# Kernel optimization log

Hardware: AMD Instinct MI355X
Metric: run time of the kernel (lower is better)

## Reference

```python
import jax, jax.numpy as jnp
import numpy as np

B, L, A, BD, K, M, FP, R, T = 256, 128, 39, 10, 6, 256, 256, 3, 2


def _gru(x, h, w_ih, w_hh, b_ih, b_hh):
    # PyTorch GRUCell: gates ordered (reset, update, new)
    gi = x @ w_ih.T + b_ih
    gh = h @ w_hh.T + b_hh
    i_r, i_z, i_n = jnp.split(gi, 3, axis=-1)
    h_r, h_z, h_n = jnp.split(gh, 3, axis=-1)
    r = jax.nn.sigmoid(i_r + h_r)
    z = jax.nn.sigmoid(i_z + h_z)
    n = jnp.tanh(i_n + r * h_n)
    return (1.0 - z) * n + z * h


def setup_inputs() -> dict:
    key = jax.random.key(0)
    ks = jax.random.split(key, 26)
    n = lambda i, shape: jax.random.normal(ks[i], shape, jnp.float32) * 0.05
    return dict(
        atom_list=jax.random.normal(ks[0], (B, L, A), jnp.float32),
        bond_list=jax.random.normal(ks[1], (B, M, BD), jnp.float32),
        atom_degree_list=jax.random.randint(ks[2], (B, L, K), 0, L),
        bond_degree_list=jax.random.randint(ks[3], (B, L, K), 0, M),
        atom_mask=jnp.ones((B, L), jnp.float32),
        atom_fc_W=n(4, (FP, A)), atom_fc_b=n(5, (FP,)),
        neighbor_fc_W=n(6, (FP, A + BD)), neighbor_fc_b=n(7, (FP,)),
        gru_w_ih=n(8, (R, 3 * FP, FP)), gru_w_hh=n(9, (R, 3 * FP, FP)),
        gru_b_ih=n(10, (R, 3 * FP)), gru_b_hh=n(11, (R, 3 * FP)),
        align_W=n(12, (R, 1, 2 * FP)), align_b=n(13, (R, 1)),
        attend_W=n(14, (R, FP, FP)), attend_b=n(15, (R, FP)),
        mol_gru_w_ih=n(16, (3 * FP, FP)), mol_gru_w_hh=n(17, (3 * FP, FP)),
        mol_gru_b_ih=n(18, (3 * FP,)), mol_gru_b_hh=n(19, (3 * FP,)),
        mol_align_W=n(20, (1, 2 * FP)), mol_align_b=n(21, (1,)),
        mol_attend_W=n(22, (FP, FP)), mol_attend_b=n(23, (FP,)),
    )


def reference(atom_list, bond_list, atom_degree_list, bond_degree_list, atom_mask,
              atom_fc_W, atom_fc_b, neighbor_fc_W, neighbor_fc_b,
              gru_w_ih, gru_w_hh, gru_b_ih, gru_b_hh,
              align_W, align_b, attend_W, attend_b,
              mol_gru_w_ih, mol_gru_w_hh, mol_gru_b_ih, mol_gru_b_hh,
              mol_align_W, mol_align_b, mol_attend_W, mol_attend_b):
    Bn, Ln, _ = atom_list.shape
    Fp = atom_fc_W.shape[0]
    gather = jax.vmap(lambda t, i: t[i])  # per-batch row gather

    atom_pre = atom_list @ atom_fc_W.T + atom_fc_b          # (B,L,FP) pre-relu
    atom_feature = jax.nn.relu(atom_pre)
    afv = [atom_pre]

    bond_neighbor = gather(bond_list, bond_degree_list)      # (B,L,K,BD)
    atom_neighbor = gather(atom_list, atom_degree_list)      # (B,L,K,A)
    nf = jax.nn.relu(jnp.concatenate([atom_neighbor, bond_neighbor], -1)
                     @ neighbor_fc_W.T + neighbor_fc_b)       # (B,L,K,FP)

    pad = atom_degree_list == Ln - 1                          # padding-atom index
    attend_mask = jnp.where(pad, 0.0, 1.0)[..., None]
    softmax_mask = jnp.where(pad, -9.0, 0.0)[..., None]

    h = atom_feature.reshape(Bn * Ln, Fp)
    act = atom_feature
    awv = []
    for d in range(R):
        neigh = nf if d == 0 else gather(act, atom_degree_list)
        fa = jnp.concatenate(
            [jnp.broadcast_to(act[:, :, None, :], neigh.shape), neigh], -1)
        score = jax.nn.relu(fa @ align_W[d].T + align_b[d]) + softmax_mask
        aw = jax.nn.softmax(score, axis=-2) * attend_mask     # (B,L,K,1)
        awv.append(aw)
        ctx = jax.nn.relu(jnp.sum(aw * (neigh @ attend_W[d].T + attend_b[d]), -2))
        h = _gru(ctx.reshape(Bn * Ln, Fp), h,
                 gru_w_ih[d], gru_w_hh[d], gru_b_ih[d], gru_b_hh[d])
        atom_feature = h.reshape(Bn, Ln, Fp)
        act = jax.nn.relu(atom_feature)
        afv.append(act)

    m3 = atom_mask[..., None]
    mol_unb = [jnp.sum(atom_feature * m3, -2)]
    mol_feature = jnp.sum(act * m3, -2)
    act_mol = jax.nn.relu(mol_feature)
    mfv = [mol_feature]
    mawv = []
    mol_smask = jnp.where(m3 == 0, -9e8, 0.0)
    for _ in range(T):
        ma = jnp.concatenate(
            [jnp.broadcast_to(act_mol[:, None, :], act.shape), act], -1)
        ms = jax.nn.relu(ma @ mol_align_W.T + mol_align_b) + mol_smask
        mw = jax.nn.softmax(ms, axis=-2) * m3                 # (B,L,1)
        mawv.append(mw)
        mctx = jax.nn.relu(jnp.sum(mw * (act @ mol_attend_W.T + mol_attend_b), -2))
        mol_feature = _gru(mctx, mol_feature,
                           mol_gru_w_ih, mol_gru_w_hh, mol_gru_b_ih, mol_gru_b_hh)
        mol_unb.append(mol_feature)
        act_mol = jax.nn.relu(mol_feature)
        mfv.append(act_mol)

    return (atom_feature, jnp.stack(afv), jnp.stack(awv), jnp.stack(mfv),
            jnp.stack(mol_unb), jnp.stack(mawv), mol_feature)
```

## Files before the change

kernel.cpp:

```cpp
#include <hip/hip_runtime.h>
#include <hip/hip_bf16.h>

#define BB 256
#define LL 128
#define AA 39
#define BDD 10
#define KK 6
#define MM 256
#define FP 256
#define RR 3
#define TT 2

using short8  = __attribute__((ext_vector_type(8))) short;
using short4v = __attribute__((ext_vector_type(4))) short;
using f32x4   = __attribute__((ext_vector_type(4))) float;
using f32x2   = __attribute__((ext_vector_type(2))) float;

__device__ __forceinline__ short f2bf(float f) {
    union { float f; unsigned u; } v; v.f = f;
    unsigned u = v.u;
    u += 0x7fffu + ((u >> 16) & 1u);
    return (short)(u >> 16);
}
__device__ __forceinline__ float bf2f(short s) {
    union { unsigned u; float f; } v; v.u = ((unsigned)(unsigned short)s) << 16;
    return v.f;
}
__device__ __forceinline__ float wred64(float v) {
#pragma unroll
    for (int off = 32; off >= 1; off >>= 1) v += __shfl_xor(v, off);
    return v;
}

#define GLL(gp, lp) __builtin_amdgcn_global_load_lds( \
    (const __attribute__((address_space(1))) void*)(gp), \
    (__attribute__((address_space(3))) void*)(lp), 16, 0, 0)

__global__ __launch_bounds__(256) void k_transpose(const float* __restrict__ src,
                                                   float* __restrict__ dst, int O, int I) {
    int idx = blockIdx.x * 256 + threadIdx.x;
    if (idx >= O * I) return;
    int o = idx / I, i = idx - o * I;
    dst[i * O + o] = src[idx];
}

__global__ __launch_bounds__(256) void k_prep_gruw(const float* __restrict__ gwih,
                                                   const float* __restrict__ gwhh,
                                                   short* __restrict__ out) {
    int idx = blockIdx.x * 256 + threadIdx.x;
    if (idx >= RR * 2 * 8 * 48 * 512) return;
    int j = idx & 7;
    int lane = (idx >> 3) & 63;
    int blk = idx >> 9;
    int nt = blk % 48;
    int ks = (blk / 48) % 8;
    int mat = (blk / (48 * 8)) % 2;
    int d = blk / (48 * 8 * 2);
    int n = nt * 16 + (lane & 15);
    int k = ks * 32 + (lane >> 4) * 8 + j;
    const float* W = mat ? gwhh : gwih;
    out[idx] = f2bf(W[((size_t)d * 768 + n) * FP + k]);
}

__global__ __launch_bounds__(256) void k_prep_molfrag(const float* __restrict__ mih,
                                                      const float* __restrict__ mhh,
                                                      short* __restrict__ out) {
    int idx = blockIdx.x * 256 + threadIdx.x;
    if (idx >= 2 * 8 * 48 * 512) return;
    int j = idx & 7;
    int lane = (idx >> 3) & 63;
    int blk = idx >> 9;
    int nt = blk % 48;
    int ks = (blk / 48) % 8;
    int mat = blk / (48 * 8);
    int n = nt * 16 + (lane & 15);
    int k = ks * 32 + (lane >> 4) * 8 + j;
    const float* W = mat ? mhh : mih;
    out[idx] = f2bf(W[(size_t)n * FP + k]);
}

__global__ __launch_bounds__(256) void k_prep_waf(const float* __restrict__ atW,
                                                  short* __restrict__ out) {
    int idx = blockIdx.x * 256 + threadIdx.x;
    if (idx >= RR * 8 * 16 * 512) return;
    int j = idx & 7;
    int lane = (idx >> 3) & 63;
    int blk = idx >> 9;
    int nt = blk % 16;
    int ks = (blk / 16) % 8;
    int d = blk / 128;
    int n = nt * 16 + (lane & 15);
    int k = ks * 32 + (lane >> 4) * 8 + j;
    out[idx] = f2bf(atW[(size_t)d * FP * FP + (size_t)n * FP + k]);
}

__global__ __launch_bounds__(256) void k_atom_pre(const float* __restrict__ atom_list,
                                                  const float* __restrict__ WafcT,
                                                  const float* __restrict__ afc_b,
                                                  const float* __restrict__ WnT,
                                                  const float* __restrict__ bn,
                                                  float* __restrict__ out_pre,
                                                  short* __restrict__ hb16,
                                                  short* __restrict__ ApreB) {
    int g0 = blockIdx.x * 8;
    int t = threadIdx.x;
    __shared__ float x[8][AA];
    for (int i = t; i < 8 * AA; i += 256) x[i / AA][i % AA] = atom_list[(size_t)g0 * AA + i];
    __syncthreads();
    float a1[8], a2[8];
    float b1 = afc_b[t], b2 = bn[t];
#pragma unroll
    for (int a = 0; a < 8; ++a) { a1[a] = b1; a2[a] = b2; }
    for (int i = 0; i < AA; ++i) {
        float w1 = WafcT[i * FP + t];
        float w2 = WnT[i * FP + t];
#pragma unroll
        for (int a = 0; a < 8; ++a) { a1[a] += x[a][i] * w1; a2[a] += x[a][i] * w2; }
    }
#pragma unroll
    for (int a = 0; a < 8; ++a) {
        size_t idx = (size_t)(g0 + a) * FP + t;
        out_pre[idx] = a1[a];
        hb16[idx] = f2bf(fmaxf(a1[a], 0.f));
        ApreB[idx] = f2bf(a2[a]);
    }
}

__global__ __launch_bounds__(512) void k_actx_d0(
        const short* __restrict__ ACTB,
        const short* __restrict__ ApreB,
        const float* __restrict__ bond_list,
        const int* __restrict__ adeg, const int* __restrict__ bdeg,
        const float* __restrict__ WnT,
        const float* __restrict__ alW, const float* __restrict__ alb,
        const short* __restrict__ WaF, const float* __restrict__ atb,
        short* __restrict__ ctx_out, float* __restrict__ awv_out) {
    __shared__ __align__(16) short aS[32768];
    __shared__ __align__(16) short cS[32768];
    __shared__ int jxS[LL * KK];
    __shared__ int bxS[LL * KK];
    __shared__ float swS[LL];

    const int b = blockIdx.x;
    const int t = threadIdx.x;
    const int wave = t >> 6, lane = t & 63;
    const int lr = lane & 15, lk = lane >> 4;

#define SLAB_OFF(r, cb) ((((r) * 512 + (cb))) ^ ((((r) & 7)) << 4))
#define A4R(r, c)  (*(const short4v*)((const char*)aS + SLAB_OFF(r, (c) * 2)))
#define C8R(r, c)  (*(const short8*)((const char*)cS + SLAB_OFF(r, (c) * 2)))
#define CW4(r, c, v) (*(short4v*)((char*)cS + SLAB_OFF(r, (c) * 2)) = (v))

    {
        const char* src = (const char*)(ApreB + (size_t)b * LL * FP);
#pragma unroll
        for (int it = 0; it < 8; ++it) {
            int off = it * 8192 + wave * 1024 + lane * 16;
            int so = off ^ (((off >> 9) & 7) << 4);
            GLL(src + so, (char*)aS + off);
        }
        for (int i = t; i < LL * KK; i += 512) {
            jxS[i] = adeg[b * LL * KK + i];
            bxS[i] = bdeg[b * LL * KK + i];
        }
    }

    f32x4 w0 = *(const f32x4*)(alW + lane * 4);
    f32x4 w1 = *(const f32x4*)(alW + FP + lane * 4);
    float bias = alb[0];

    float wnt[BDD][4];
#pragma unroll
    for (int i = 0; i < BDD; ++i) {
        f32x4 v = *(const f32x4*)(WnT + (AA + i) * FP + lane * 4);
#pragma unroll
        for (int q = 0; q < 4; ++q) wnt[i][q] = v[q];
    }
    __syncthreads();

    for (int ai = 0; ai < 16; ++ai) {
        const int a = wave * 16 + ai;
        const int ga = b * LL + a;

        short4v sv = *(const short4v*)(ACTB + (size_t)ga * FP + lane * 4);
        float ss = wred64(bf2f(sv[0]) * w0[0] + bf2f(sv[1]) * w0[1] +
                          bf2f(sv[2]) * w0[2] + bf2f(sv[3]) * w0[3]);

        int jx[KK];
#pragma unroll
        for (int k = 0; k < KK; ++k) jx[k] = jxS[a * KK + k];

        float nf[KK][4];
        float sc[KK];
#pragma unroll
        for (int k = 0; k < KK; ++k) {
            short4v nv = A4R(jx[k], lane * 4);
            float f0 = bf2f(nv[0]), f1 = bf2f(nv[1]), f2 = bf2f(nv[2]), f3 = bf2f(nv[3]);
            int bi = bxS[a * KK + k];
            const float* bp = bond_list + ((size_t)b * MM + bi) * BDD;
            float bb[BDD];
#pragma unroll
            for (int i = 0; i < 5; ++i) {
                f32x2 v2 = *(const f32x2*)(bp + 2 * i);
                bb[2 * i] = v2[0]; bb[2 * i + 1] = v2[1];
            }
            float b0 = 0.f, b1 = 0.f, b2 = 0.f, b3 = 0.f;
#pragma unroll
            for (int i = 0; i < BDD; ++i) {
                b0 += bb[i] * wnt[i][0]; b1 += bb[i] * wnt[i][1];
                b2 += bb[i] * wnt[i][2]; b3 += bb[i] * wnt[i][3];
            }
            f0 = fmaxf(f0 + b0, 0.f); f1 = fmaxf(f1 + b1, 0.f);
            f2 = fmaxf(f2 + b2, 0.f); f3 = fmaxf(f3 + b3, 0.f);
            nf[k][0] = f0; nf[k][1] = f1; nf[k][2] = f2; nf[k][3] = f3;
            float s2 = wred64(f0 * w1[0] + f1 * w1[1] + f2 * w1[2] + f3 * w1[3]);
            float s = fmaxf(ss + s2 + bias, 0.f);
            if (jx[k] == LL - 1) s -= 9.0f;
            sc[k] = s;
        }

        float m = sc[0];
#pragma unroll
        for (int k = 1; k < KK; ++k) m = fmaxf(m, sc[k]);
        float e[KK], den = 0.f;
#pragma unroll
        for (int k = 0; k < KK; ++k) { e[k] = expf(sc[k] - m); den += e[k]; }
        float aw[KK], sumaw = 0.f;
#pragma unroll
        for (int k = 0; k < KK; ++k) {
            aw[k] = (jx[k] == LL - 1) ? 0.f : e[k] / den;
            sumaw += aw[k];
        }
        if (lane < KK) {
            float av = aw[0];
#pragma unroll
            for (int k = 1; k < KK; ++k) if (lane == k) av = aw[k];
            awv_out[(size_t)ga * KK + lane] = av;
        }
        if (lane == 0) swS[a] = sumaw;

        short4v wo;
#pragma unroll
        for (int q = 0; q < 4; ++q) {
            float w = 0.f;
#pragma unroll
            for (int k = 0; k < KK; ++k) w += aw[k] * nf[k][q];
            wo[q] = f2bf(w);
        }
        CW4(a, lane * 4, wo);
    }
    __syncthreads();

    {
        const int rg = wave >> 1, csl = wave & 1;
        f32x4 acc[2][8] = {};
        const short8* wb = (const short8*)WaF;
        for (int ks = 0; ks < 8; ++ks) {
            short8 a0 = C8R(rg * 32 + lr, ks * 32 + lk * 8);
            short8 a1 = C8R(rg * 32 + 16 + lr, ks * 32 + lk * 8);
#pragma unroll
            for (int nt2 = 0; nt2 < 8; ++nt2) {
                short8 bf = wb[(size_t)(ks * 16 + csl * 8 + nt2) * 64 + lane];
                acc[0][nt2] = __builtin_amdgcn_mfma_f32_16x16x32_bf16(a0, bf, acc[0][nt2], 0, 0, 0);
                acc[1][nt2] = __builtin_amdgcn_mfma_f32_16x16x32_bf16(a1, bf, acc[1][nt2], 0, 0, 0);
            }
        }
#pragma unroll
        for (int rt = 0; rt < 2; ++rt)
#pragma unroll
        for (int nt2 = 0; nt2 < 8; ++nt2) {
            int col = csl * 128 + nt2 * 16 + lr;
            float abv = atb[col];
#pragma unroll
            for (int q = 0; q < 4; ++q) {
                int row = rg * 32 + rt * 16 + lk * 4 + q;
                float v = acc[rt][nt2][q] + swS[row] * abv;
                ctx_out[((size_t)b * LL + row) * FP + col] = f2bf(fmaxf(v, 0.f));
            }
        }
    }
#undef SLAB_OFF
#undef A4R
#undef C8R
#undef CW4
}

__global__ __launch_bounds__(512) void k_actx(int d,
        const short* __restrict__ ACTB,
        const int* __restrict__ adeg,
        const float* __restrict__ alW, const float* __restrict__ alb,
        const short* __restrict__ WaF, const float* __restrict__ atb,
        short* __restrict__ ctx_out, float* __restrict__ awv_out) {
    __shared__ __align__(16) short aS[32768];
    __shared__ __align__(16) short cS[32768];
    __shared__ int   jxS[LL * KK];
    __shared__ float awS[LL * KK];
    __shared__ float swS[LL];

    const int b = blockIdx.x;
    const int t = threadIdx.x;
    const int wave = t >> 6, lane = t & 63;
    const int lr = lane & 15, lk = lane >> 4;

#define SLAB_OFF(r, cb) ((((r) * 512 + (cb))) ^ ((((r) & 7)) << 4))
#define A4R(r, c)  (*(const short4v*)((const char*)aS + SLAB_OFF(r, (c) * 2)))
#define C8R(r, c)  (*(const short8*)((const char*)cS + SLAB_OFF(r, (c) * 2)))
#define CW4(r, c, v) (*(short4v*)((char*)cS + SLAB_OFF(r, (c) * 2)) = (v))

    {
        const char* src = (const char*)(ACTB + (size_t)b * LL * FP);
#pragma unroll
        for (int it = 0; it < 8; ++it) {
            int off = it * 8192 + wave * 1024 + lane * 16;
            int so = off ^ (((off >> 9) & 7) << 4);
            GLL(src + so, (char*)aS + off);
        }
        for (int i = t; i < LL * KK; i += 512) jxS[i] = adeg[b * LL * KK + i];
    }
    __syncthreads();

    {
        f32x4 w0 = *(const f32x4*)(alW + (size_t)d * 2 * FP + lane * 4);
        f32x4 w1 = *(const f32x4*)(alW + (size_t)d * 2 * FP + FP + lane * 4);
        float bias = alb[d];
        for (int ai = 0; ai < 16; ++ai) {
            int a = wave * 16 + ai;
            short4v sv = A4R(a, lane * 4);
            float ss = wred64(bf2f(sv[0]) * w0[0] + bf2f(sv[1]) * w0[1] +
                              bf2f(sv[2]) * w0[2] + bf2f(sv[3]) * w0[3]);
            float sc[KK]; int jx[KK];
#pragma unroll
            for (int k = 0; k < KK; ++k) {
                int j = jxS[a * KK + k]; jx[k] = j;
                short4v nv = A4R(j, lane * 4);
                float s2 = wred64(bf2f(nv[0]) * w1[0] + bf2f(nv[1]) * w1[1] +
                                  bf2f(nv[2]) * w1[2] + bf2f(nv[3]) * w1[3]);
                float s = fmaxf(ss + s2 + bias, 0.f);
                if (j == LL - 1) s -= 9.0f;
                sc[k] = s;
            }
            float m = sc[0];
#pragma unroll
            for (int k = 1; k < KK; ++k) m = fmaxf(m, sc[k]);
            float e[KK], den = 0.f;
#pragma unroll
            for (int k = 0; k < KK; ++k) { e[k] = expf(sc[k] - m); den += e[k]; }
            float aw[KK], sumaw = 0.f;
#pragma unroll
            for (int k = 0; k < KK; ++k) {
                aw[k] = (jx[k] == LL - 1) ? 0.f : e[k] / den;
                sumaw += aw[k];
            }
            if (lane < KK) {
                float av = aw[0];
#pragma unroll
                for (int k = 1; k < KK; ++k) if (lane == k) av = aw[k];
                awS[a * KK + lane] = av;
                awv_out[((size_t)b * LL + a) * KK + lane] = av;
            }
            if (lane == 0) swS[a] = sumaw;
        }
    }
    __syncthreads();

    for (int ai = 0; ai < 16; ++ai) {
        int a = wave * 16 + ai;
        float a0 = 0.f, a1 = 0.f, a2 = 0.f, a3 = 0.f;
#pragma unroll
        for (int k = 0; k < KK; ++k) {
            float awv = awS[a * KK + k];
            short4v nv = A4R(jxS[a * KK + k], lane * 4);
            a0 += awv * bf2f(nv[0]);
            a1 += awv * bf2f(nv[1]);
            a2 += awv * bf2f(nv[2]);
            a3 += awv * bf2f(nv[3]);
        }
        short4v wo; wo[0] = f2bf(a0); wo[1] = f2bf(a1); wo[2] = f2bf(a2); wo[3] = f2bf(a3);
        CW4(a, lane * 4, wo);
    }
    __syncthreads();

    {
        const int rg = wave >> 1, csl = wave & 1;
        f32x4 acc[2][8] = {};
        const short8* wb = (const short8*)(WaF + (size_t)d * 8 * 16 * 512);
        for (int ks = 0; ks < 8; ++ks) {
            short8 a0 = C8R(rg * 32 + lr, ks * 32 + lk * 8);
            short8 a1 = C8R(rg * 32 + 16 + lr, ks * 32 + lk * 8);
#pragma unroll
            for (int nt2 = 0; nt2 < 8; ++nt2) {
                short8 bf = wb[(size_t)(ks * 16 + csl * 8 + nt2) * 64 + lane];
                acc[0][nt2] = __builtin_amdgcn_mfma_f32_16x16x32_bf16(a0, bf, acc[0][nt2], 0, 0, 0);
                acc[1][nt2] = __builtin_amdgcn_mfma_f32_16x16x32_bf16(a1, bf, acc[1][nt2], 0, 0, 0);
            }
        }
#pragma unroll
        for (int rt = 0; rt < 2; ++rt)
#pragma unroll
        for (int nt2 = 0; nt2 < 8; ++nt2) {
            int col = csl * 128 + nt2 * 16 + lr;
            float abv = atb[d * FP + col];
#pragma unroll
            for (int q = 0; q < 4; ++q) {
                int row = rg * 32 + rt * 16 + lk * 4 + q;
                float v = acc[rt][nt2][q] + swS[row] * abv;
                ctx_out[((size_t)b * LL + row) * FP + col] = f2bf(fmaxf(v, 0.f));
            }
        }
    }
#undef SLAB_OFF
#undef A4R
#undef C8R
#undef CW4
}

template<int LAST>
__global__ __launch_bounds__(512) void k_gru_mfma(
        const short* __restrict__ XB,
        const short* __restrict__ HBl,
        float* __restrict__ hbuf,
        const short* __restrict__ Bih,
        const short* __restrict__ Bhh,
        const float* __restrict__ bih, const float* __restrict__ bhh,
        float* __restrict__ act_out,
        short* __restrict__ HB_out,
        short* __restrict__ ACT_out) {
    __shared__ short ldsB[3][12288];
    __shared__ short ldsA[2][16384];
    const int t = threadIdx.x;
    const int wave = t >> 6, lane = t & 63;
    const int rh = wave >> 2;
    const int wn = wave & 3;
    const int lr = lane & 15, lk = lane >> 4;
    const int bid = blockIdx.x;
    const int kofs = bid & 7;
    const int abase = bid * 64;

#define PKS(p)  ((((p) >> 2) + kofs) & 7)
#define STAGEP(p) do { \
        const short* base_ = ((((p) >> 1) & 1) ? Bhh : Bih) + (size_t)PKS(p) * 24576; \
        const int h_ = (p) & 1; \
        _Pragma("unroll") \
        for (int e = 0; e < 3; ++e) { \
            int j = wave * 3 + e; \
            int nt = 4 * (j >> 1) + 2 * h_ + (j & 1); \
            GLL(base_ + nt * 512 + lane * 8, &ldsB[(p) % 3][j * 512]); \
        } } while (0)
#define LDA_READ(s, r, c) (*(const short8*)((const char*)ldsA[s] + \
        ((((r) * 512 + (c) * 2)) ^ ((((r) & 7)) << 4))))
#define LDA_READ1(s, r, c) (*(const short*)((const char*)ldsA[s] + \
        ((((r) * 512 + (c) * 2)) ^ ((((r) & 7)) << 4))))

    {
        const char* xsrc = (const char*)(XB + (size_t)abase * FP);
        const char* hsrc = (const char*)(HBl + (size_t)abase * FP);
#pragma unroll
        for (int it = 0; it < 4; ++it) {
            int off = it * 8192 + wave * 1024 + lane * 16;
            int src = off ^ (((off >> 9) & 7) << 4);
            GLL(xsrc + src, (char*)ldsA[0] + off);
            GLL(hsrc + src, (char*)ldsA[1] + off);
        }
    }
    STAGEP(0);
    STAGEP(1);

    f32x4 acc_rz[2][8] = {};
    f32x4 acc_in[2][4] = {};
    f32x4 acc_hn[2][4] = {};

    short8 ax0{}, ah0{}, ax1{}, ah1{};
#pragma unroll
    for (int p = 0; p < 32; ++p) {
        if (p < 31) { asm volatile("s_waitcnt vmcnt(3)" ::: "memory"); }
        else        { asm volatile("s_waitcnt vmcnt(0)" ::: "memory"); }
        __builtin_amdgcn_s_barrier();
        __builtin_amdgcn_sched_barrier(0);
        if (p < 30) STAGEP(p + 2);
        const int h_ = p & 1;
        const int mat = (p >> 1) & 1;
        if ((p & 3) == 0) {
            int ks = PKS(p);
            int c = ks * 32 + lk * 8;
            ax0 = LDA_READ(0, rh * 32 + lr, c);
            ah0 = LDA_READ(1, rh * 32 + lr, c);
            ax1 = LDA_READ(0, rh * 32 + 16 + lr, c);
            ah1 = LDA_READ(1, rh * 32 + 16 + lr, c);
        }
#pragma unroll
        for (int rg = 0; rg < 2; ++rg) {
            const short8 a8 = mat ? (rg ? ah1 : ah0) : (rg ? ax1 : ax0);
#pragma unroll
            for (int g = 0; g < 3; ++g) {
#pragma unroll
                for (int s2 = 0; s2 < 2; ++s2) {
                    const int sub = 2 * h_ + s2;
                    const int j = ((4 * g + wn) << 1) | s2;
                    short8 bf = *(const short8*)(&ldsB[p % 3][j * 512 + lane * 8]);
                    if (g < 2)
                        acc_rz[rg][g * 4 + sub] = __builtin_amdgcn_mfma_f32_16x16x32_bf16(a8, bf, acc_rz[rg][g * 4 + sub], 0, 0, 0);
                    else if (mat)
                        acc_hn[rg][sub] = __builtin_amdgcn_mfma_f32_16x16x32_bf16(a8, bf, acc_hn[rg][sub], 0, 0, 0);
                    else
                        acc_in[rg][sub] = __builtin_amdgcn_mfma_f32_16x16x32_bf16(a8, bf, acc_in[rg][sub], 0, 0, 0);
                }
            }
        }
    }
#undef STAGEP
#undef PKS

#pragma unroll
    for (int sub = 0; sub < 4; ++sub) {
        int c = wn * 64 + sub * 16 + lr;
        float brz_r = bih[c] + bhh[c];
        float brz_z = bih[FP + c] + bhh[FP + c];
        float bin_ = bih[2 * FP + c];
        float bhn = bhh[2 * FP + c];
#pragma unroll
        for (int rg = 0; rg < 2; ++rg) {
#pragma unroll
            for (int q = 0; q < 4; ++q) {
                int row = rh * 32 + rg * 16 + lk * 4 + q;
                int atom = abase + row;
                size_t idx = (size_t)atom * FP + c;
                float hold = bf2f(LDA_READ1(1, row, c));
                float r = 1.f / (1.f + expf(-(acc_rz[rg][0 * 4 + sub][q] + brz_r)));
                float z = 1.f / (1.f + expf(-(acc_rz[rg][1 * 4 + sub][q] + brz_z)));
                float n = tanhf(acc_in[rg][sub][q] + bin_ + r * (acc_hn[rg][sub][q] + bhn));
                float hn = (1.f - z) * n + z * hold;
                float rl = fmaxf(hn, 0.f);
                act_out[idx] = rl;
                if constexpr (LAST) {
                    hbuf[idx] = hn;
                } else {
                    HB_out[idx] = f2bf(hn);
                    ACT_out[idx] = f2bf(rl);
                }
            }
        }
    }
#undef LDA_READ
#undef LDA_READ1
}

__global__ __launch_bounds__(256) void k_mol_reduce(const float* __restrict__ hbuf,
                                                    const float* __restrict__ act,
                                                    const float* __restrict__ mask,
                                                    const float* __restrict__ malW,
                                                    float* __restrict__ o_unb0,
                                                    float* __restrict__ o_mfv0,
                                                    float* __restrict__ molF,
                                                    short* __restrict__ MOLFb,
                                                    float* __restrict__ S2g) {
    int b = blockIdx.x, t = threadIdx.x;
    int wave = t >> 6, lane = t & 63;
    float s1 = 0.f, s2 = 0.f;
    for (int l = 0; l < LL; ++l) {
        float mk = mask[b * LL + l];
        s1 += hbuf[((size_t)b * LL + l) * FP + t] * mk;
        s2 += act[((size_t)b * LL + l) * FP + t] * mk;
    }
    o_unb0[b * FP + t] = s1;
    o_mfv0[b * FP + t] = s2;
    molF[b * FP + t] = s2;
    MOLFb[b * FP + t] = f2bf(s2);

    for (int l = wave; l < LL; l += 4) {
        float v2 = 0.f;
#pragma unroll
        for (int q = 0; q < 4; ++q) {
            int i = lane + 64 * q;
            v2 += act[((size_t)b * LL + l) * FP + i] * malW[FP + i];
        }
        v2 = wred64(v2);
        if (lane == 0) S2g[b * LL + l] = v2;
    }
}

__global__ __launch_bounds__(256) void k_mstep(int step,
        const float* __restrict__ act,
        const float* __restrict__ molF,
        const float* __restrict__ mask,
        const float* __restrict__ S2g,
        const float* __restrict__ malW, const float* __restrict__ malb,
        const float* __restrict__ MWaT, const float* __restrict__ matb,
        short* __restrict__ MCTXb,
        float* __restrict__ o_mawv) {
    int b = blockIdx.x, t = threadIdx.x;
    int wave = t >> 6, lane = t & 63;
    __shared__ float sS[LL], mwS[LL], waS[FP];
    __shared__ float red[4];

    float hprev = molF[b * FP + t];
    float am = fmaxf(hprev, 0.f);

    float v = am * malW[t];
    v = wred64(v);
    if (lane == 0) red[wave] = v;
    __syncthreads();
    float s_self = red[0] + red[1] + red[2] + red[3];

    if (t < LL) {
        float s = fmaxf(s_self + S2g[b * LL + t] + malb[0], 0.f);
        if (mask[b * LL + t] == 0.f) s += -9e8f;
        sS[t] = s;
    }
    __syncthreads();

    float m = -1e30f;
    for (int l = 0; l < LL; ++l) m = fmaxf(m, sS[l]);
    float den = 0.f;
    for (int l = 0; l < LL; ++l) den += expf(sS[l] - m);
    if (t < LL) {
        float w = expf(sS[t] - m) / den * mask[b * LL + t];
        mwS[t] = w;
        o_mawv[(size_t)step * (BB * LL) + b * LL + t] = w;
    }
    __syncthreads();

    float sumaw = 0.f;
    for (int l = 0; l < LL; ++l) sumaw += mwS[l];

    float wa = 0.f;
    for (int l = 0; l < LL; ++l) wa += mwS[l] * act[((size_t)b * LL + l) * FP + t];
    waS[t] = wa;
    __syncthreads();

    float acc = sumaw * matb[t];
    for (int i = 0; i < FP; ++i) acc += waS[i] * MWaT[i * FP + t];
    MCTXb[b * FP + t] = f2bf(fmaxf(acc, 0.f));
}

__global__ __launch_bounds__(512) void k_mol_gru(int step,
        const short* __restrict__ XB,
        const short* __restrict__ HBl,
        const short* __restrict__ Bih,
        const short* __restrict__ Bhh,
        const float* __restrict__ bih, const float* __restrict__ bhh,
        float* __restrict__ o_unb, float* __restrict__ o_mfv,
        float* __restrict__ molF, short* __restrict__ MOLFb,
        float* __restrict__ o_molfeat) {
    __shared__ short ldsB[3][12288];
    __shared__ short ldsA[2][16384];
    const int t = threadIdx.x;
    const int wave = t >> 6, lane = t & 63;
    const int rh = wave >> 2;
    const int wn = wave & 3;
    const int lr = lane & 15, lk = lane >> 4;
    const int bid = blockIdx.x;
    const int kofs = bid & 7;
    const int abase = bid * 64;

#define PKS(p)  ((((p) >> 2) + kofs) & 7)
#define STAGEP(p) do { \
        const short* base_ = ((((p) >> 1) & 1) ? Bhh : Bih) + (size_t)PKS(p) * 24576; \
        const int h_ = (p) & 1; \
        _Pragma("unroll") \
        for (int e = 0; e < 3; ++e) { \
            int j = wave * 3 + e; \
            int nt = 4 * (j >> 1) + 2 * h_ + (j & 1); \
            GLL(base_ + nt * 512 + lane * 8, &ldsB[(p) % 3][j * 512]); \
        } } while (0)
#define LDA_READ(s, r, c) (*(const short8*)((const char*)ldsA[s] + \
        ((((r) * 512 + (c) * 2)) ^ ((((r) & 7)) << 4))))
#define LDA_READ1(s, r, c) (*(const short*)((const char*)ldsA[s] + \
        ((((r) * 512 + (c) * 2)) ^ ((((r) & 7)) << 4))))

    {
        const char* xsrc = (const char*)(XB + (size_t)abase * FP);
        const char* hsrc = (const char*)(HBl + (size_t)abase * FP);
#pragma unroll
        for (int it = 0; it < 4; ++it) {
            int off = it * 8192 + wave * 1024 + lane * 16;
            int src = off ^ (((off >> 9) & 7) << 4);
            GLL(xsrc + src, (char*)ldsA[0] + off);
            GLL(hsrc + src, (char*)ldsA[1] + off);
        }
    }
    STAGEP(0);
    STAGEP(1);

    f32x4 acc_rz[2][8] = {};
    f32x4 acc_in[2][4] = {};
    f32x4 acc_hn[2][4] = {};

    short8 ax0{}, ah0{}, ax1{}, ah1{};
#pragma unroll
    for (int p = 0; p < 32; ++p) {
        if (p < 31) { asm volatile("s_waitcnt vmcnt(3)" ::: "memory"); }
        else        { asm volatile("s_waitcnt vmcnt(0)" ::: "memory"); }
        __builtin_amdgcn_s_barrier();
        __builtin_amdgcn_sched_barrier(0);
        if (p < 30) STAGEP(p + 2);
        const int h_ = p & 1;
        const int mat = (p >> 1) & 1;
        if ((p & 3) == 0) {
            int ks = PKS(p);
            int c = ks * 32 + lk * 8;
            ax0 = LDA_READ(0, rh * 32 + lr, c);
            ah0 = LDA_READ(1, rh * 32 + lr, c);
            ax1 = LDA_READ(0, rh * 32 + 16 + lr, c);
            ah1 = LDA_READ(1, rh * 32 + 16 + lr, c);
        }
#pragma unroll
        for (int rg = 0; rg < 2; ++rg) {
            const short8 a8 = mat ? (rg ? ah1 : ah0) : (rg ? ax1 : ax0);
#pragma unroll
            for (int g = 0; g < 3; ++g) {
#pragma unroll
                for (int s2 = 0; s2 < 2; ++s2) {
                    const int sub = 2 * h_ + s2;
                    const int j = ((4 * g + wn) << 1) | s2;
                    short8 bf = *(const short8*)(&ldsB[p % 3][j * 512 + lane * 8]);
                    if (g < 2)
                        acc_rz[rg][g * 4 + sub] = __builtin_amdgcn_mfma_f32_16x16x32_bf16(a8, bf, acc_rz[rg][g * 4 + sub], 0, 0, 0);
                    else if (mat)
                        acc_hn[rg][sub] = __builtin_amdgcn_mfma_f32_16x16x32_bf16(a8, bf, acc_hn[rg][sub], 0, 0, 0);
                    else
                        acc_in[rg][sub] = __builtin_amdgcn_mfma_f32_16x16x32_bf16(a8, bf, acc_in[rg][sub], 0, 0, 0);
                }
            }
        }
    }
#undef STAGEP
#undef PKS

#pragma unroll
    for (int sub = 0; sub < 4; ++sub) {
        int c = wn * 64 + sub * 16 + lr;
        float brz_r = bih[c] + bhh[c];
        float brz_z = bih[FP + c] + bhh[FP + c];
        float bin_ = bih[2 * FP + c];
        float bhn = bhh[2 * FP + c];
#pragma unroll
        for (int rg = 0; rg < 2; ++rg) {
#pragma unroll
            for (int q = 0; q < 4; ++q) {
                int row = rh * 32 + rg * 16 + lk * 4 + q;
                int m = abase + row;
                size_t idx = (size_t)m * FP + c;
                float hold = bf2f(LDA_READ1(1, row, c));
                float r = 1.f / (1.f + expf(-(acc_rz[rg][0 * 4 + sub][q] + brz_r)));
                float z = 1.f / (1.f + expf(-(acc_rz[rg][1 * 4 + sub][q] + brz_z)));
                float n = tanhf(acc_in[rg][sub][q] + bin_ + r * (acc_hn[rg][sub][q] + bhn));
                float hn = (1.f - z) * n + z * hold;
                o_unb[(size_t)(step + 1) * (BB * FP) + idx] = hn;
                o_mfv[(size_t)(step + 1) * (BB * FP) + idx] = fmaxf(hn, 0.f);
                molF[idx] = hn;
                MOLFb[idx] = f2bf(hn);
                if (step == TT - 1) o_molfeat[idx] = hn;
            }
        }
    }
#undef LDA_READ
#undef LDA_READ1
}

extern "C" void kernel_launch(void* const* d_in, const int* in_sizes, int n_in,
                              void* d_out, int out_size, void* d_ws, size_t ws_size,
                              hipStream_t stream) {
    const float* atom_list = (const float*)d_in[0];
    const float* bond_list = (const float*)d_in[1];
    const int*   adeg      = (const int*)d_in[2];
    const int*   bdeg      = (const int*)d_in[3];
    const float* amask     = (const float*)d_in[4];
    const float* atom_fc_W = (const float*)d_in[5];
    const float* atom_fc_b = (const float*)d_in[6];
    const float* nfc_W     = (const float*)d_in[7];
    const float* nfc_b     = (const float*)d_in[8];
    const float* gwih      = (const float*)d_in[9];
    const float* gwhh      = (const float*)d_in[10];
    const float* gbih      = (const float*)d_in[11];
    const float* gbhh      = (const float*)d_in[12];
    const float* alW       = (const float*)d_in[13];
    const float* alb       = (const float*)d_in[14];
    const float* atW       = (const float*)d_in[15];
    const float* atb       = (const float*)d_in[16];
    const float* mgwih     = (const float*)d_in[17];
    const float* mgwhh     = (const float*)d_in[18];
    const float* mgbih     = (const float*)d_in[19];
    const float* mgbhh     = (const float*)d_in[20];
    const float* malW      = (const float*)d_in[21];
    const float* malb      = (const float*)d_in[22];
    const float* matW      = (const float*)d_in[23];
    const float* matb      = (const float*)d_in[24];

    const size_t BLF = (size_t)BB * LL * FP;
    float* out = (float*)d_out;
    float* O0 = out;
    float* O1 = out + BLF;
    float* O2 = O1 + 4 * BLF;
    float* O3 = O2 + (size_t)RR * BB * LL * KK;
    float* O4 = O3 + (size_t)(TT + 1) * BB * FP;
    float* O5 = O4 + (size_t)(TT + 1) * BB * FP;
    float* O6 = O5 + (size_t)TT * BB * LL;

    float* ws = (float*)d_ws;
    short* XB   = (short*)ws;
    short* XB2  = XB + BLF;
    short* HBb  = XB + 2 * BLF;
    short* ACTB = XB + 3 * BLF;
    float* rest = ws + 2 * BLF;
    short* ApreB = (short*)rest;
    float* SW    = rest + BLF / 2;
    float* MOLF  = SW + (size_t)BB * LL;
    float* WafcT = MOLF + (size_t)BB * FP;
    float* WnT   = WafcT + AA * FP;
    float* MWaT  = WnT + (AA + BDD) * FP;
    short* MolGW = (short*)(MWaT + (size_t)FP * FP);
    short* GW    = MolGW + (size_t)2 * 8 * 48 * 512;
    short* WaF   = GW + (size_t)RR * 2 * 8 * 48 * 512;
    short* MCTXb = WaF + (size_t)RR * 8 * 16 * 512;
    short* MOLFb = MCTXb + (size_t)BB * FP;
    float* S2g   = (float*)(MOLFb + (size_t)BB * FP);
    (void)ws_size; (void)in_sizes; (void)n_in; (void)out_size;

    auto tr = [&](const float* src, float* dst, int O, int I) {
        int n = O * I;
        k_transpose<<<(n + 255) / 256, 256, 0, stream>>>(src, dst, O, I);
    };
    tr(atom_fc_W, WafcT, FP, AA);
    tr(nfc_W, WnT, FP, AA + BDD);
    tr(matW, MWaT, FP, FP);

    {
        int n = RR * 2 * 8 * 48 * 512;
        k_prep_gruw<<<(n + 255) / 256, 256, 0, stream>>>(gwih, gwhh, GW);
        int n2 = RR * 8 * 16 * 512;
        k_prep_waf<<<(n2 + 255) / 256, 256, 0, stream>>>(atW, WaF);
        int n3 = 2 * 8 * 48 * 512;
        k_prep_molfrag<<<(n3 + 255) / 256, 256, 0, stream>>>(mgwih, mgwhh, MolGW);
    }

    k_atom_pre<<<BB * LL / 8, 256, 0, stream>>>(atom_list, WafcT, atom_fc_b,
                                                WnT, nfc_b, O1, HBb, ApreB);

    const size_t wblk = (size_t)8 * 48 * 512;
    for (int d = 0; d < RR; ++d) {
        if (d == 0) {
            k_actx_d0<<<BB, 512, 0, stream>>>(HBb, ApreB, bond_list, adeg, bdeg,
                    WnT, alW, alb, WaF, atb, XB2, O2);
        } else {
            k_actx<<<BB, 512, 0, stream>>>(d, ACTB, adeg,
                    alW, alb, WaF, atb,
                    XB2, O2 + (size_t)d * BB * LL * KK);
        }
        if (d == RR - 1) {
            k_gru_mfma<1><<<BB * LL / 64, 512, 0, stream>>>(XB2, HBb, O0,
                    GW + (size_t)(d * 2 + 0) * wblk, GW + (size_t)(d * 2 + 1) * wblk,
                    gbih + (size_t)d * 768, gbhh + (size_t)d * 768,
                    O1 + (size_t)(d + 1) * BLF, HBb, ACTB);
        } else {
            k_gru_mfma<0><<<BB * LL / 64, 512, 0, stream>>>(XB2, HBb, O0,
                    GW + (size_t)(d * 2 + 0) * wblk, GW + (size_t)(d * 2 + 1) * wblk,
                    gbih + (size_t)d * 768, gbhh + (size_t)d * 768,
                    O1 + (size_t)(d + 1) * BLF, HBb, ACTB);
        }
    }

    const float* actFin = O1 + (size_t)RR * BLF;
    k_mol_reduce<<<BB, 256, 0, stream>>>(O0, actFin, amask, malW,
                                         O4, O3, MOLF, MOLFb, S2g);
    for (int st = 0; st < TT; ++st) {
        k_mstep<<<BB, 256, 0, stream>>>(st, actFin, MOLF, amask, S2g,
                malW, malb, MWaT, matb, MCTXb, O5);
        k_mol_gru<<<4, 512, 0, stream>>>(st, MCTXb, MOLFb,
                MolGW, MolGW + wblk, mgbih, mgbhh,
                O4, O3, MOLF, MOLFb, O6);
    }
}
```

Baseline: 541.2 us.

## Fuse prep kernels, merge actx attention passes, fold first mol step into reduce

Merges the three transpose launches into one and the three weight-pack launches into one. In k_actx, alignment softmax and weighted neighbor sum now run in a single pass, keeping neighbor rows in registers instead of re-reading LDS and dropping the awS buffer and one barrier. The first molecule attention step is folded into the reduce kernel, which removes one launch. Fewer launches and less LDS traffic in exchange for higher register pressure and a serial per-block tail in the mol head.

```diff
diff --git a/kernel.cpp b/kernel.cpp
--- a/kernel.cpp
+++ b/kernel.cpp
@@ -36,62 +36,58 @@
     (const __attribute__((address_space(1))) void*)(gp), \
     (__attribute__((address_space(3))) void*)(lp), 16, 0, 0)
 
-__global__ __launch_bounds__(256) void k_transpose(const float* __restrict__ src,
-                                                   float* __restrict__ dst, int O, int I) {
+__global__ __launch_bounds__(256) void k_prep_trans(
+        const float* __restrict__ atom_fc_W, const float* __restrict__ nfc_W,
+        const float* __restrict__ matW,
+        float* __restrict__ WafcT, float* __restrict__ WnT, float* __restrict__ MWaT) {
+    const int N1 = FP * AA, N2 = FP * (AA + BDD), N3 = FP * FP;
     int idx = blockIdx.x * 256 + threadIdx.x;
-    if (idx >= O * I) return;
-    int o = idx / I, i = idx - o * I;
-    dst[i * O + o] = src[idx];
-}
-
-__global__ __launch_bounds__(256) void k_prep_gruw(const float* __restrict__ gwih,
-                                                   const float* __restrict__ gwhh,
-                                                   short* __restrict__ out) {
+    if (idx < N1) {
+        int o = idx / AA, i = idx - o * AA;
+        WafcT[i * FP + o] = atom_fc_W[idx];
+    } else if (idx < N1 + N2) {
+        int r = idx - N1;
+        int o = r / (AA + BDD), i = r - o * (AA + BDD);
+        WnT[i * FP + o] = nfc_W[r];
+    } else if (idx < N1 + N2 + N3) {
+        int r = idx - N1 - N2;
+        int o = r >> 8, i = r & 255;
+        MWaT[i * FP + o] = matW[r];
+    }
+}
+
+__global__ __launch_bounds__(256) void k_prep_pack(
+        const float* __restrict__ gwih, const float* __restrict__ gwhh,
+        const float* __restrict__ atW,
+        const float* __restrict__ mih, const float* __restrict__ mhh,
+        short* __restrict__ GW, short* __restrict__ WaF, short* __restrict__ MolGW) {
+    const int N1 = RR * 2 * 8 * 48 * 512;
+    const int N2 = RR * 8 * 16 * 512;
+    const int N3 = 2 * 8 * 48 * 512;
     int idx = blockIdx.x * 256 + threadIdx.x;
-    if (idx >= RR * 2 * 8 * 48 * 512) return;
-    int j = idx & 7;
-    int lane = (idx >> 3) & 63;
-    int blk = idx >> 9;
-    int nt = blk % 48;
-    int ks = (blk / 48) % 8;
-    int mat = (blk / (48 * 8)) % 2;
-    int d = blk / (48 * 8 * 2);
-    int n = nt * 16 + (lane & 15);
-    int k = ks * 32 + (lane >> 4) * 8 + j;
-    const float* W = mat ? gwhh : gwih;
-    out[idx] = f2bf(W[((size_t)d * 768 + n) * FP + k]);
-}
-
-__global__ __launch_bounds__(256) void k_prep_molfrag(const float* __restrict__ mih,
-                                                      const float* __restrict__ mhh,
-                                                      short* __restrict__ out) {
-    int idx = blockIdx.x * 256 + threadIdx.x;
-    if (idx >= 2 * 8 * 48 * 512) return;
-    int j = idx & 7;
-    int lane = (idx >> 3) & 63;
-    int blk = idx >> 9;
-    int nt = blk % 48;
-    int ks = (blk / 48) % 8;
-    int mat = blk / (48 * 8);
-    int n = nt * 16 + (lane & 15);
-    int k = ks * 32 + (lane >> 4) * 8 + j;
-    const float* W = mat ? mhh : mih;
-    out[idx] = f2bf(W[(size_t)n * FP + k]);
-}
-
-__global__ __launch_bounds__(256) void k_prep_waf(const float* __restrict__ atW,
-                                                  short* __restrict__ out) {
-    int idx = blockIdx.x * 256 + threadIdx.x;
-    if (idx >= RR * 8 * 16 * 512) return;
-    int j = idx & 7;
-    int lane = (idx >> 3) & 63;
-    int blk = idx >> 9;
-    int nt = blk % 16;
-    int ks = (blk / 16) % 8;
-    int d = blk / 128;
-    int n = nt * 16 + (lane & 15);
-    int k = ks * 32 + (lane >> 4) * 8 + j;
-    out[idx] = f2bf(atW[(size_t)d * FP * FP + (size_t)n * FP + k]);
+    if (idx < N1) {
+        int j = idx & 7, lane = (idx >> 3) & 63, blk = idx >> 9;
+        int nt = blk % 48, ks = (blk / 48) % 8, mat = (blk / 384) % 2, d = blk / 768;
+        int n = nt * 16 + (lane & 15);
+        int k = ks * 32 + (lane >> 4) * 8 + j;
+        const float* W = mat ? gwhh : gwih;
+        GW[idx] = f2bf(W[((size_t)d * 768 + n) * FP + k]);
+    } else if (idx < N1 + N2) {
+        int r = idx - N1;
+        int j = r & 7, lane = (r >> 3) & 63, blk = r >> 9;
+        int nt = blk % 16, ks = (blk / 16) % 8, d = blk / 128;
+        int n = nt * 16 + (lane & 15);
+        int k = ks * 32 + (lane >> 4) * 8 + j;
+        WaF[r] = f2bf(atW[(size_t)d * FP * FP + (size_t)n * FP + k]);
+    } else if (idx < N1 + N2 + N3) {
+        int r = idx - N1 - N2;
+        int j = r & 7, lane = (r >> 3) & 63, blk = r >> 9;
+        int nt = blk % 48, ks = (blk / 48) % 8, mat = blk / 384;
+        int n = nt * 16 + (lane & 15);
+        int k = ks * 32 + (lane >> 4) * 8 + j;
+        const float* W = mat ? mhh : mih;
+        MolGW[r] = f2bf(W[(size_t)n * FP + k]);
+    }
 }
 
 __global__ __launch_bounds__(256) void k_atom_pre(const float* __restrict__ atom_list,
@@ -294,7 +290,6 @@
     __shared__ __align__(16) short aS[32768];
     __shared__ __align__(16) short cS[32768];
     __shared__ int   jxS[LL * KK];
-    __shared__ float awS[LL * KK];
     __shared__ float swS[LL];
 
     const int b = blockIdx.x;
@@ -317,65 +312,66 @@
         }
         for (int i = t; i < LL * KK; i += 512) jxS[i] = adeg[b * LL * KK + i];
     }
-    __syncthreads();
-
-    {
-        f32x4 w0 = *(const f32x4*)(alW + (size_t)d * 2 * FP + lane * 4);
-        f32x4 w1 = *(const f32x4*)(alW + (size_t)d * 2 * FP + FP + lane * 4);
-        float bias = alb[d];
-        for (int ai = 0; ai < 16; ++ai) {
-            int a = wave * 16 + ai;
-            short4v sv = A4R(a, lane * 4);
-            float ss = wred64(bf2f(sv[0]) * w0[0] + bf2f(sv[1]) * w0[1] +
-                              bf2f(sv[2]) * w0[2] + bf2f(sv[3]) * w0[3]);
-            float sc[KK]; int jx[KK];
-#pragma unroll
-            for (int k = 0; k < KK; ++k) {
-                int j = jxS[a * KK + k]; jx[k] = j;
-                short4v nv = A4R(j, lane * 4);
-                float s2 = wred64(bf2f(nv[0]) * w1[0] + bf2f(nv[1]) * w1[1] +
-                                  bf2f(nv[2]) * w1[2] + bf2f(nv[3]) * w1[3]);
-                float s = fmaxf(ss + s2 + bias, 0.f);
-                if (j == LL - 1) s -= 9.0f;
-                sc[k] = s;
-            }
-            float m = sc[0];
-#pragma unroll
-            for (int k = 1; k < KK; ++k) m = fmaxf(m, sc[k]);
-            float e[KK], den = 0.f;
-#pragma unroll
-            for (int k = 0; k < KK; ++k) { e[k] = expf(sc[k] - m); den += e[k]; }
-            float aw[KK], sumaw = 0.f;
-#pragma unroll
-            for (int k = 0; k < KK; ++k) {
-                aw[k] = (jx[k] == LL - 1) ? 0.f : e[k] / den;
-                sumaw += aw[k];
-            }
-            if (lane < KK) {
-                float av = aw[0];
-#pragma unroll
-                for (int k = 1; k < KK; ++k) if (lane == k) av = aw[k];
-                awS[a * KK + lane] = av;
-                awv_out[((size_t)b * LL + a) * KK + lane] = av;
-            }
-            if (lane == 0) swS[a] = sumaw;
-        }
-    }
+
+    f32x4 w0 = *(const f32x4*)(alW + (size_t)d * 2 * FP + lane * 4);
+    f32x4 w1 = *(const f32x4*)(alW + (size_t)d * 2 * FP + FP + lane * 4);
+    float bias = alb[d];
     __syncthreads();
 
     for (int ai = 0; ai < 16; ++ai) {
-        int a = wave * 16 + ai;
-        float a0 = 0.f, a1 = 0.f, a2 = 0.f, a3 = 0.f;
+        const int a = wave * 16 + ai;
+        const int ga = b * LL + a;
+
+        short4v sv = A4R(a, lane * 4);
+        float ss = wred64(bf2f(sv[0]) * w0[0] + bf2f(sv[1]) * w0[1] +
+                          bf2f(sv[2]) * w0[2] + bf2f(sv[3]) * w0[3]);
+
+        int jx[KK];
+#pragma unroll
+        for (int k = 0; k < KK; ++k) jx[k] = jxS[a * KK + k];
+
+        float nf[KK][4];
+        float sc[KK];
 #pragma unroll
         for (int k = 0; k < KK; ++k) {
-            float awv = awS[a * KK + k];
-            short4v nv = A4R(jxS[a * KK + k], lane * 4);
-            a0 += awv * bf2f(nv[0]);
-            a1 += awv * bf2f(nv[1]);
-            a2 += awv * bf2f(nv[2]);
-            a3 += awv * bf2f(nv[3]);
-        }
-        short4v wo; wo[0] = f2bf(a0); wo[1] = f2bf(a1); wo[2] = f2bf(a2); wo[3] = f2bf(a3);
+            short4v nv = A4R(jx[k], lane * 4);
+            nf[k][0] = bf2f(nv[0]); nf[k][1] = bf2f(nv[1]);
+            nf[k][2] = bf2f(nv[2]); nf[k][3] = bf2f(nv[3]);
+            float s2 = wred64(nf[k][0] * w1[0] + nf[k][1] * w1[1] +
+                              nf[k][2] * w1[2] + nf[k][3] * w1[3]);
+            float s = fmaxf(ss + s2 + bias, 0.f);
+            if (jx[k] == LL - 1) s -= 9.0f;
+            sc[k] = s;
+        }
+
+        float m = sc[0];
+#pragma unroll
+        for (int k = 1; k < KK; ++k) m = fmaxf(m, sc[k]);
+        float e[KK], den = 0.f;
+#pragma unroll
+        for (int k = 0; k < KK; ++k) { e[k] = expf(sc[k] - m); den += e[k]; }
+        float aw[KK], sumaw = 0.f;
+#pragma unroll
+        for (int k = 0; k < KK; ++k) {
+            aw[k] = (jx[k] == LL - 1) ? 0.f : e[k] / den;
+            sumaw += aw[k];
+        }
+        if (lane < KK) {
+            float av = aw[0];
+#pragma unroll
+            for (int k = 1; k < KK; ++k) if (lane == k) av = aw[k];
+            awv_out[(size_t)ga * KK + lane] = av;
+        }
+        if (lane == 0) swS[a] = sumaw;
+
+        short4v wo;
+#pragma unroll
+        for (int q = 0; q < 4; ++q) {
+            float w = 0.f;
+#pragma unroll
+            for (int k = 0; k < KK; ++k) w += aw[k] * nf[k][q];
+            wo[q] = f2bf(w);
+        }
         CW4(a, lane * 4, wo);
     }
     __syncthreads();
@@ -544,17 +540,20 @@
 #undef LDA_READ1
 }
 
-__global__ __launch_bounds__(256) void k_mol_reduce(const float* __restrict__ hbuf,
-                                                    const float* __restrict__ act,
-                                                    const float* __restrict__ mask,
-                                                    const float* __restrict__ malW,
-                                                    float* __restrict__ o_unb0,
-                                                    float* __restrict__ o_mfv0,
-                                                    float* __restrict__ molF,
-                                                    short* __restrict__ MOLFb,
-                                                    float* __restrict__ S2g) {
+__global__ __launch_bounds__(256) void k_mol_head(
+        const float* __restrict__ hbuf, const float* __restrict__ act,
+        const float* __restrict__ mask,
+        const float* __restrict__ malW, const float* __restrict__ malb,
+        const float* __restrict__ MWaT, const float* __restrict__ matb,
+        float* __restrict__ o_unb0, float* __restrict__ o_mfv0,
+        float* __restrict__ molF, short* __restrict__ MOLFb,
+        float* __restrict__ S2g,
+        short* __restrict__ MCTXb, float* __restrict__ o_mawv) {
     int b = blockIdx.x, t = threadIdx.x;
     int wave = t >> 6, lane = t & 63;
+    __shared__ float sS2[LL], sS[LL], mwS[LL], waS[FP];
+    __shared__ float red[4];
+
     float s1 = 0.f, s2 = 0.f;
     for (int l = 0; l < LL; ++l) {
         float mk = mask[b * LL + l];
@@ -574,8 +573,45 @@
             v2 += act[((size_t)b * LL + l) * FP + i] * malW[FP + i];
         }
         v2 = wred64(v2);
-        if (lane == 0) S2g[b * LL + l] = v2;
-    }
+        if (lane == 0) { sS2[l] = v2; S2g[b * LL + l] = v2; }
+    }
+
+    float am = fmaxf(s2, 0.f);
+    float v = am * malW[t];
+    v = wred64(v);
+    if (lane == 0) red[wave] = v;
+    __syncthreads();
+    float s_self = red[0] + red[1] + red[2] + red[3];
+
+    if (t < LL) {
+        float s = fmaxf(s_self + sS2[t] + malb[0], 0.f);
+        if (mask[b * LL + t] == 0.f) s += -9e8f;
+        sS[t] = s;
+    }
+    __syncthreads();
+
+    float m = -1e30f;
+    for (int l = 0; l < LL; ++l) m = fmaxf(m, sS[l]);
+    float den = 0.f;
+    for (int l = 0; l < LL; ++l) den += expf(sS[l] - m);
+    if (t < LL) {
+        float w = expf(sS[t] - m) / den * mask[b * LL + t];
+        mwS[t] = w;
+        o_mawv[b * LL + t] = w;
+    }
+    __syncthreads();
+
+    float sumaw = 0.f;
+    for (int l = 0; l < LL; ++l) sumaw += mwS[l];
+
+    float wa = 0.f;
+    for (int l = 0; l < LL; ++l) wa += mwS[l] * act[((size_t)b * LL + l) * FP + t];
+    waS[t] = wa;
+    __syncthreads();
+
+    float acc = sumaw * matb[t];
+    for (int i = 0; i < FP; ++i) acc += waS[i] * MWaT[i * FP + t];
+    MCTXb[b * FP + t] = f2bf(fmaxf(acc, 0.f));
 }
 
 __global__ __launch_bounds__(256) void k_mstep(int step,
@@ -816,21 +852,13 @@
     float* S2g   = (float*)(MOLFb + (size_t)BB * FP);
     (void)ws_size; (void)in_sizes; (void)n_in; (void)out_size;
 
-    auto tr = [&](const float* src, float* dst, int O, int I) {
-        int n = O * I;
-        k_transpose<<<(n + 255) / 256, 256, 0, stream>>>(src, dst, O, I);
-    };
-    tr(atom_fc_W, WafcT, FP, AA);
-    tr(nfc_W, WnT, FP, AA + BDD);
-    tr(matW, MWaT, FP, FP);
-
     {
-        int n = RR * 2 * 8 * 48 * 512;
-        k_prep_gruw<<<(n + 255) / 256, 256, 0, stream>>>(gwih, gwhh, GW);
-        int n2 = RR * 8 * 16 * 512;
-        k_prep_waf<<<(n2 + 255) / 256, 256, 0, stream>>>(atW, WaF);
-        int n3 = 2 * 8 * 48 * 512;
-        k_prep_molfrag<<<(n3 + 255) / 256, 256, 0, stream>>>(mgwih, mgwhh, MolGW);
+        int nT = FP * AA + FP * (AA + BDD) + FP * FP;
+        k_prep_trans<<<(nT + 255) / 256, 256, 0, stream>>>(atom_fc_W, nfc_W, matW,
+                                                           WafcT, WnT, MWaT);
+        int nP = RR * 2 * 8 * 48 * 512 + RR * 8 * 16 * 512 + 2 * 8 * 48 * 512;
+        k_prep_pack<<<(nP + 255) / 256, 256, 0, stream>>>(gwih, gwhh, atW,
+                                                          mgwih, mgwhh, GW, WaF, MolGW);
     }
 
     k_atom_pre<<<BB * LL / 8, 256, 0, stream>>>(atom_list, WafcT, atom_fc_b,
@@ -860,13 +888,14 @@
     }
 
     const float* actFin = O1 + (size_t)RR * BLF;
-    k_mol_reduce<<<BB, 256, 0, stream>>>(O0, actFin, amask, malW,
-                                         O4, O3, MOLF, MOLFb, S2g);
-    for (int st = 0; st < TT; ++st) {
-        k_mstep<<<BB, 256, 0, stream>>>(st, actFin, MOLF, amask, S2g,
-                malW, malb, MWaT, matb, MCTXb, O5);
-        k_mol_gru<<<4, 512, 0, stream>>>(st, MCTXb, MOLFb,
-                MolGW, MolGW + wblk, mgbih, mgbhh,
-                O4, O3, MOLF, MOLFb, O6);
-    }
-}
+    k_mol_head<<<BB, 256, 0, stream>>>(O0, actFin, amask, malW, malb, MWaT, matb,
+                                       O4, O3, MOLF, MOLFb, S2g, MCTXb, O5);
+    k_mol_gru<<<4, 512, 0, stream>>>(0, MCTXb, MOLFb,
+            MolGW, MolGW + wblk, mgbih, mgbhh,
+            O4, O3, MOLF, MOLFb, O6);
+    k_mstep<<<BB, 256, 0, stream>>>(1, actFin, MOLF, amask, S2g,
+            malW, malb, MWaT, matb, MCTXb, O5);
+    k_mol_gru<<<4, 512, 0, stream>>>(1, MCTXb, MOLFb,
+            MolGW, MolGW + wblk, mgbih, mgbhh,
+            O4, O3, MOLF, MOLFb, O6);
+}
```

Result: no change. 538.4 us (-0.5%).
